# Performance work log

Hardware: AMD Instinct MI355X
Metric: run time of the kernel (lower is better)

## Reference

```python
import jax, jax.numpy as jnp
import numpy as np

KMAX = 192  # static upper bound on sampled subset size k (E[k]~116, std~10 for our vals)


def _dpp_sample(vals, vecs, seed):
    """Sequential DPP sampling (Hough et al. algorithm), jit-compatible via
    fixed-width column padding (KMAX) and lax.while_loop over the k iterations.
    The original's nested classical Gram-Schmidt re-orthonormalization is
    expressed as a QR factorization with the R-diagonal sign convention of GS."""
    n = vals.shape[0]
    key = jax.random.key(seed)
    k_idx, k_loop = jax.random.split(key)

    # Bernoulli selection of eigenvectors: rand(n) < vals/(vals+1)
    index = jax.random.uniform(k_idx, (n,)) < vals / (vals + 1.0)
    k = jnp.sum(index.astype(jnp.int32))
    kk = jnp.minimum(k, KMAX)

    # Pack selected eigenvector columns to the left (stable sort: True first)
    order = jnp.argsort(~index)
    colmask0 = (jnp.arange(KMAX) < kk).astype(vals.dtype)
    V0 = vecs[:, order[:KMAX]] * colmask0[None, :]  # [n, KMAX]

    cols = jnp.arange(KMAX)

    def cond(st):
        i, V, subset = st
        return i < kk

    def body(st):
        i, V, subset = st
        m = kk - i  # number of active columns
        # p_i = ||V[i,:]||^2 over active columns (inactive cols are zero)
        p = jnp.sum(V * V, axis=1)
        c = jnp.cumsum(p / jnp.sum(p))
        u = jax.random.uniform(jax.random.fold_in(k_loop, i))
        item = jnp.argmax(u < c)  # first index where cdf exceeds u
        subset = subset.at[item].set(jnp.asarray(1.0, subset.dtype))
        # first active column j with |V[item, j]| > 0
        jmask = (jnp.abs(V[item]) > 0) & (cols < m)
        j = jnp.argmax(jmask)
        Vj = V[:, j]
        # delete column j (shift left), shrink active width to m-1
        src = jnp.minimum(jnp.where(cols >= j, cols + 1, cols), KMAX - 1)
        newmask = (cols < (m - 1)).astype(V.dtype)
        Vd = V[:, src] * newmask[None, :]
        # eliminate: V <- V - Vj * V[item,:] / Vj[item]
        Ve = (Vd - jnp.outer(Vj, Vd[item] / Vj[item])) * newmask[None, :]
        # re-orthonormalize active columns (classical GS == QR with positive R diag)
        Q, R = jnp.linalg.qr(Ve)
        d = jnp.diagonal(R)
        Q = Q * jnp.where(d >= 0, 1.0, -1.0)[None, :]
        Vn = Q * newmask[None, :]
        Vn = jnp.where(m > 1, Vn, V)  # original skips update when V has 1 column
        return (i + 1, Vn, subset)

    subset0 = jnp.zeros((n,), vals.dtype)
    _, _, subset = jax.lax.while_loop(cond, body, (jnp.int32(0), V0, subset0))
    # original returns all-ones when every eigenvector is selected
    return jnp.where(k == n, jnp.ones((n,), vals.dtype), subset)


def setup_inputs() -> dict:
    key = jax.random.key(0)
    k1, k2 = jax.random.split(key)
    n = 2048
    # eigenvalues in (0.01, 0.11) so E[|subset|] ~ 0.054*n ~ 116 << KMAX
    e = jax.random.uniform(k1, (n,), jnp.float32) * 0.1 + 0.01
    # orthonormal eigenvectors (proper eigendecomposition of a DPP kernel)
    v = jnp.linalg.qr(jax.random.normal(k2, (n, n), jnp.float32))[0]
    return {"e": e, "v": v, "seed": 0}


def reference(e, v, seed):
    return _dpp_sample(e, v, seed)
```

## Files before the change

kernel.cpp:

```cpp
#include <hip/hip_runtime.h>
#include <hip/hip_fp16.h>
#include <stdint.h>
#include <stddef.h>

#define N 2048
#define KMX 192
#define NTH 1024

typedef _Float16 f16x2 __attribute__((ext_vector_type(2)));
typedef _Float16 f16x4 __attribute__((ext_vector_type(4)));

#if defined(__has_builtin)
#if __has_builtin(__builtin_amdgcn_fdot2)
#define HAS_FDOT2 1
#endif
#endif

__device__ __forceinline__ f16x2 bch2(unsigned u) { return __builtin_bit_cast(f16x2, u); }
__device__ __forceinline__ unsigned packh2(float a, float b) {
  unsigned ua = (unsigned)__half_as_ushort(__float2half(a));
  unsigned ub = (unsigned)__half_as_ushort(__float2half(b));
  return ua | (ub << 16);
}
__device__ __forceinline__ float dot2acc(unsigned c, unsigned y, float acc) {
#ifdef HAS_FDOT2
  return __builtin_amdgcn_fdot2(bch2(c), bch2(y), acc, false);
#else
  f16x2 cv = bch2(c), yv = bch2(y);
  acc = fmaf((float)cv[0], (float)yv[0], acc);
  acc = fmaf((float)cv[1], (float)yv[1], acc);
  return acc;
#endif
}

__device__ __forceinline__ void tfround(unsigned &x0, unsigned &x1, const int d) {
  x0 += x1;
  x1 = (x1 << d) | (x1 >> (32 - d));
  x1 ^= x0;
}

__device__ __forceinline__ uint2 tf2x32(unsigned k0, unsigned k1, unsigned c0, unsigned c1) {
  unsigned ks2 = k0 ^ k1 ^ 0x1BD11BDAu;
  unsigned x0 = c0 + k0, x1 = c1 + k1;
  tfround(x0,x1,13); tfround(x0,x1,15); tfround(x0,x1,26); tfround(x0,x1,6);
  x0 += k1;  x1 += ks2 + 1u;
  tfround(x0,x1,17); tfround(x0,x1,29); tfround(x0,x1,16); tfround(x0,x1,24);
  x0 += ks2; x1 += k0 + 2u;
  tfround(x0,x1,13); tfround(x0,x1,15); tfround(x0,x1,26); tfround(x0,x1,6);
  x0 += k0;  x1 += k1 + 3u;
  tfround(x0,x1,17); tfround(x0,x1,29); tfround(x0,x1,16); tfround(x0,x1,24);
  x0 += k1;  x1 += ks2 + 4u;
  tfround(x0,x1,13); tfround(x0,x1,15); tfround(x0,x1,26); tfround(x0,x1,6);
  x0 += ks2; x1 += k0 + 5u;
  uint2 r; r.x = x0; r.y = x1;
  return r;
}

__device__ __forceinline__ float u01(unsigned bits) {
  return __uint_as_float((bits >> 9) | 0x3f800000u) - 1.0f;
}

__global__ void k_select(const float* __restrict__ e, const int* __restrict__ seedp,
                         int* __restrict__ hdr, int* __restrict__ sel) {
  __shared__ unsigned kx0, kx1;
  __shared__ int cnt_s[256];
  __shared__ int pre_s[256];
  const int tid = threadIdx.x;
  if (tid == 0) {
    unsigned seed = (unsigned)seedp[0];
    uint2 kidx  = tf2x32(0u, seed, 0u, 0u);
    uint2 kloop = tf2x32(0u, seed, 0u, 1u);
    kx0 = kidx.x; kx1 = kidx.y;
    hdr[2] = (int)kloop.x;
    hdr[3] = (int)kloop.y;
  }
  __syncthreads();
  const unsigned a0 = kx0, a1 = kx1;
  int flags = 0;
  #pragma unroll
  for (int r = 0; r < 8; ++r) {
    const int i = tid * 8 + r;
    uint2 o = tf2x32(a0, a1, 0u, (unsigned)i);
    float u = u01(o.x ^ o.y);
    float ev = e[i];
    float thr = ev / (ev + 1.0f);
    if (u < thr) flags |= (1 << r);
  }
  cnt_s[tid] = __popc(flags);
  __syncthreads();
  if (tid == 0) {
    int acc = 0;
    for (int t2 = 0; t2 < 256; ++t2) { pre_s[t2] = acc; acc += cnt_s[t2]; }
    hdr[1] = acc;
    hdr[0] = acc < KMX ? acc : KMX;
  }
  __syncthreads();
  int off = pre_s[tid];
  #pragma unroll
  for (int r = 0; r < 8; ++r) {
    if (flags & (1 << r)) {
      if (off < KMX) sel[off] = tid * 8 + r;
      ++off;
    }
  }
}

__global__ void k_gather_h(const float* __restrict__ v, const int* __restrict__ hdr,
                           const int* __restrict__ sel, __half* __restrict__ Gh) {
  const int j = blockIdx.y;
  const int i = blockIdx.x * 256 + threadIdx.x;
  float val = 0.f;
  if (j < hdr[0]) val = v[(size_t)i * N + sel[j]];
  Gh[j * N + i] = __float2half(val);
}

__global__ void k_gather(const float* __restrict__ v, const int* __restrict__ hdr,
                         const int* __restrict__ sel, float* __restrict__ G,
                         __half* __restrict__ Gh) {
  const int j = blockIdx.y;
  const int i = blockIdx.x * 256 + threadIdx.x;
  float val = 0.f;
  if (j < hdr[0]) val = v[(size_t)i * N + sel[j]];
  G[j * N + i] = val;
  Gh[j * N + i] = __float2half(val);
}

__global__ void __launch_bounds__(256)
k_gram(const __half* __restrict__ Gh, const int* __restrict__ hdr,
       __half* __restrict__ Kh) {
  __shared__ __align__(16) __half As[32][64];
  __shared__ __align__(16) __half Bs[32][64];
  const int tid = threadIdx.x;
  const int i0 = blockIdx.y * 64;
  const int i1 = blockIdx.x * 64;
  const int tr = tid & 15, tc = tid >> 4;
  const int kk = hdr[0];
  int kc = (kk + 31) & ~31;
  if (kc > KMX) kc = KMX;

  float acc[4][4];
  #pragma unroll
  for (int r = 0; r < 4; ++r)
    #pragma unroll
    for (int c = 0; c < 4; ++c) acc[r][c] = 0.f;

  const int jr = tid >> 3, c8 = (tid & 7) * 8;
  for (int j0 = 0; j0 < kc; j0 += 32) {
    *(uint4*)&As[jr][c8] = *(const uint4*)(Gh + (size_t)(j0 + jr) * N + i0 + c8);
    *(uint4*)&Bs[jr][c8] = *(const uint4*)(Gh + (size_t)(j0 + jr) * N + i1 + c8);
    __syncthreads();
    #pragma unroll 8
    for (int k = 0; k < 32; ++k) {
      f16x4 a4 = *(const f16x4*)&As[k][tr * 4];
      f16x4 b4 = *(const f16x4*)&Bs[k][tc * 4];
      #pragma unroll
      for (int r = 0; r < 4; ++r)
        #pragma unroll
        for (int c = 0; c < 4; ++c)
          acc[r][c] = fmaf((float)a4[r], (float)b4[c], acc[r][c]);
    }
    __syncthreads();
  }
  #pragma unroll
  for (int r = 0; r < 4; ++r) {
    const int row = i0 + tr * 4 + r;
    uint2 w;
    w.x = packh2(acc[r][0], acc[r][1]);
    w.y = packh2(acc[r][2], acc[r][3]);
    *(uint2*)(Kh + (size_t)row * N + i1 + tc * 4) = w;
  }
}

__global__ void __launch_bounds__(NTH)
k_dpp_chol(const int* __restrict__ hdr, const __half* __restrict__ Kh,
           uint2* __restrict__ YQ, float* __restrict__ out) {
  __shared__ float p_s[N];
  __shared__ uint2 cpack_s[KMX / 4];
  __shared__ float u_s[KMX];
  __shared__ float wsum_s[16];
  __shared__ int item_sh;

  const int tid  = threadIdx.x;
  const int lane = tid & 63;
  const int wave = tid >> 6;
  const int kk    = hdr[0];
  const int kfull = hdr[1];
  const unsigned kl0 = (unsigned)hdr[2];
  const unsigned kl1 = (unsigned)hdr[3];

  const float fill = (kfull == N) ? 1.0f : 0.0f;
  out[tid] = fill;
  out[tid + NTH] = fill;
  if (kfull == N || kk == 0) return;

  const int i0 = 2 * tid;

  float p0 = (float)Kh[(size_t)i0 * N + i0];
  float p1 = (float)Kh[(size_t)(i0 + 1) * N + i0 + 1];
  p_s[i0]     = p0;
  p_s[i0 + 1] = p1;
  if (tid < KMX) {
    uint2 fk = tf2x32(kl0, kl1, 0u, (unsigned)tid);
    uint2 ob = tf2x32(fk.x, fk.y, 0u, 0u);
    u_s[tid] = u01(ob.x ^ ob.y);
  }
  if (tid == 0) item_sh = N;
  __syncthreads();

  for (int t = 0; t < kk; ++t) {
    float ts = p0 + p1;
    float ws = ts;
    #pragma unroll
    for (int d = 1; d < 64; d <<= 1) {
      float o = __shfl_up(ws, d, 64);
      if (lane >= d) ws += o;
    }
    if (lane == 63) wsum_s[wave] = ws;
    __syncthreads();
    float wv = (lane < 16) ? wsum_s[lane] : 0.f;
    #pragma unroll
    for (int d = 1; d < 16; d <<= 1) {
      float o = __shfl_up(wv, d, 16);
      if ((lane & 15) >= d) wv += o;
    }
    const float S    = __shfl(wv, 15, 64);
    const float binc = __shfl(wv, wave, 64);
    const float base_wave = binc - wsum_s[wave];
    const float Sinv = 1.0f / S;
    const float u = u_s[t];
    float excl = __shfl_up(ws, 1, 64);
    if (lane == 0) excl = 0.f;
    const float base = base_wave + excl;
    const float c0 = (base + p0) * Sinv;
    const float c1 = (base + ts) * Sinv;
    const bool m0 = (u < c0);
    const bool m1 = (u < c1);
    unsigned long long bal = __ballot(m0 || m1);
    if (bal) {
      int first = (int)__builtin_ctzll(bal);
      if (lane == first) atomicMin(&item_sh, m0 ? i0 : i0 + 1);
    }
    __syncthreads();
    int item = item_sh;
    if (item >= N) item = 0;
    if (tid == 0) out[item] = 1.0f;
    if (t == kk - 1) break;

    const unsigned kp = *(const unsigned*)(Kh + (size_t)item * N + i0);
    const float rinv = 1.0f / sqrtf(fmaxf(p_s[item], 1e-30f));

    if (tid * 4 < t) {
      uint2 cu = YQ[(size_t)tid * N + item];
      const int rem2 = t - 4 * tid;
      if (rem2 < 4) {
        if (rem2 == 1)      { cu.x &= 0x0000FFFFu; cu.y = 0u; }
        else if (rem2 == 2) { cu.y = 0u; }
        else                { cu.y &= 0x0000FFFFu; }
      }
      cpack_s[tid] = cu;
    }
    if (tid == 0) item_sh = N;
    __syncthreads();

    {
      const int nq = (t + 3) >> 2;
      float acc0 = 0.f, acc1 = 0.f;
      const uint2* Yp = YQ + i0;
      #pragma unroll 4
      for (int q = 0; q < nq; ++q) {
        uint2 cs = cpack_s[q];
        uint4 yv = *(const uint4*)(Yp + (size_t)q * N);
        acc0 = dot2acc(cs.x, yv.x, acc0);
        acc0 = dot2acc(cs.y, yv.y, acc0);
        acc1 = dot2acc(cs.x, yv.z, acc1);
        acc1 = dot2acc(cs.y, yv.w, acc1);
      }
      f16x2 kv = bch2(kp);
      const float y0 = ((float)kv[0] - acc0) * rinv;
      const float y1 = ((float)kv[1] - acc1) * rinv;
      p0 = fmaxf(p0 - y0 * y0, 0.f);
      p1 = fmaxf(p1 - y1 * y1, 0.f);
      p_s[i0]     = p0;
      p_s[i0 + 1] = p1;
      unsigned short* Ys = (unsigned short*)YQ;
      const int rem = t & 3;
      const size_t eb = ((size_t)(t >> 2) * N + i0) * 4;
      Ys[eb + rem]     = __half_as_ushort(__float2half(y0));
      Ys[eb + 4 + rem] = __half_as_ushort(__float2half(y1));
    }
  }
}

__global__ void __launch_bounds__(NTH)
k_dpp_main(const int* __restrict__ hdr, const float* __restrict__ G,
           const __half* __restrict__ Gh, float* __restrict__ D,
           float* __restrict__ out) {
  __shared__ float p_s[N];
  __shared__ float g_s[KMX];
  __shared__ float part[16 * KMX];
  __shared__ float u_s[KMX];
  __shared__ float wsum_s[16];
  __shared__ int item_sh;

  const int tid  = threadIdx.x;
  const int lane = tid & 63;
  const int wave = tid >> 6;
  const int kk    = hdr[0];
  const int kfull = hdr[1];
  const unsigned kl0 = (unsigned)hdr[2];
  const unsigned kl1 = (unsigned)hdr[3];

  const float fill = (kfull == N) ? 1.0f : 0.0f;
  out[tid] = fill;
  out[tid + NTH] = fill;
  if (kfull == N || kk == 0) return;

  const int kkr = (kk + 15) & ~15;

  {
    float s0a = 0.f, s0b = 0.f, s1a = 0.f, s1b = 0.f;
    const __half* base = Gh + 2 * tid;
    for (int j = 0; j < kkr; j += 4) {
      float2 f0 = __half22float2(*(const __half2*)(base + (j + 0) * N));
      float2 f1 = __half22float2(*(const __half2*)(base + (j + 1) * N));
      float2 f2 = __half22float2(*(const __half2*)(base + (j + 2) * N));
      float2 f3 = __half22float2(*(const __half2*)(base + (j + 3) * N));
      s0a = fmaf(f0.x, f0.x, s0a); s1a = fmaf(f0.y, f0.y, s1a);
      s0b = fmaf(f1.x, f1.x, s0b); s1b = fmaf(f1.y, f1.y, s1b);
      s0a = fmaf(f2.x, f2.x, s0a); s1a = fmaf(f2.y, f2.y, s1a);
      s0b = fmaf(f3.x, f3.x, s0b); s1b = fmaf(f3.y, f3.y, s1b);
    }
    p_s[2 * tid]     = s0a + s0b;
    p_s[2 * tid + 1] = s1a + s1b;
    if (tid < KMX) {
      uint2 fk = tf2x32(kl0, kl1, 0u, (unsigned)tid);
      uint2 ob = tf2x32(fk.x, fk.y, 0u, 0u);
      u_s[tid] = u01(ob.x ^ ob.y);
    }
    if (tid == 0) item_sh = N;
  }
  __syncthreads();

  for (int t = 0; t < kk; ++t) {
    float a  = p_s[2 * tid];
    float b  = p_s[2 * tid + 1];
    float ts = a + b;
    float ws = ts;
    #pragma unroll
    for (int d = 1; d < 64; d <<= 1) {
      float o = __shfl_up(ws, d, 64);
      if (lane >= d) ws += o;
    }
    if (lane == 63) wsum_s[wave] = ws;
    __syncthreads();
    float S = 0.f, base_wave = 0.f;
    #pragma unroll
    for (int w = 0; w < 16; ++w) {
      float wv = wsum_s[w];
      if (w < wave) base_wave += wv;
      S += wv;
    }
    const float u = u_s[t];
    float excl = __shfl_up(ws, 1, 64);
    if (lane == 0) excl = 0.f;
    const float base = base_wave + excl;
    const float c0 = (base + a) / S;
    const float c1 = (base + ts) / S;
    const bool m0 = (u < c0);
    const bool m1 = (u < c1);
    unsigned long long bal = __ballot(m0 || m1);
    if (bal) {
      int first = (int)__builtin_ctzll(bal);
      if (lane == first) atomicMin(&item_sh, m0 ? 2 * tid : 2 * tid + 1);
    }
    __syncthreads();
    int item = item_sh;
    if (item >= N) item = 0;
    if (tid == 0) out[item] = 1.0f;
    if (t == kk - 1) break;

    if (tid < KMX) g_s[tid] = G[tid * N + item];
    __syncthreads();

    {
      float g0 = g_s[lane], g1 = g_s[lane + 64], g2 = g_s[lane + 128];
      float a0 = 0.f, a1 = 0.f, a2 = 0.f;
      for (int s = wave; s < t; s += 16) {
        const float* Dr = D + s * KMX;
        float d0 = Dr[lane], d1 = Dr[lane + 64], d2 = Dr[lane + 128];
        float acc = fmaf(d0, g0, fmaf(d1, g1, d2 * g2));
        #pragma unroll
        for (int m = 1; m < 64; m <<= 1) acc += __shfl_xor(acc, m, 64);
        a0 = fmaf(acc, d0, a0); a1 = fmaf(acc, d1, a1); a2 = fmaf(acc, d2, a2);
      }
      part[wave * KMX + lane]       = a0;
      part[wave * KMX + lane + 64]  = a1;
      part[wave * KMX + lane + 128] = a2;
    }
    __syncthreads();
    if (tid < KMX) {
      float gg = g_s[tid];
      #pragma unroll
      for (int w = 0; w < 16; ++w) gg -= part[w * KMX + tid];
      g_s[tid] = gg;
    }
    __syncthreads();

    float gg2 = 0.f;
    {
      float g0 = g_s[lane], g1 = g_s[lane + 64], g2 = g_s[lane + 128];
      float a0 = 0.f, a1 = 0.f, a2 = 0.f;
      for (int s = wave; s < t; s += 16) {
        const float* Dr = D + s * KMX;
        float d0 = Dr[lane], d1 = Dr[lane + 64], d2 = Dr[lane + 128];
        float acc = fmaf(d0, g0, fmaf(d1, g1, d2 * g2));
        #pragma unroll
        for (int m = 1; m < 64; m <<= 1) acc += __shfl_xor(acc, m, 64);
        a0 = fmaf(acc, d0, a0); a1 = fmaf(acc, d1, a1); a2 = fmaf(acc, d2, a2);
      }
      part[wave * KMX + lane]       = a0;
      part[wave * KMX + lane + 64]  = a1;
      part[wave * KMX + lane + 128] = a2;
    }
    __syncthreads();
    if (tid < KMX) {
      float gg = g_s[tid];
      #pragma unroll
      for (int w = 0; w < 16; ++w) gg -= part[w * KMX + tid];
      gg2 = gg;
    }
    if (wave < 3) {
      float r = gg2 * gg2;
      #pragma unroll
      for (int m = 1; m < 64; m <<= 1) r += __shfl_xor(r, m, 64);
      if (lane == 0) wsum_s[wave] = r;
    }
    __syncthreads();
    const float rho = sqrtf(wsum_s[0] + wsum_s[1] + wsum_s[2]);
    if (tid < KMX) {
      float dj = gg2 / rho;
      g_s[tid] = dj;
      D[t * KMX + tid] = dj;
    }
    if (tid == 0) item_sh = N;
    __syncthreads();

    {
      float s0a = 0.f, s0b = 0.f, s1a = 0.f, s1b = 0.f;
      const __half* base2 = Gh + 2 * tid;
      for (int j = 0; j < kkr; j += 4) {
        float d0 = g_s[j], d1 = g_s[j + 1], d2 = g_s[j + 2], d3 = g_s[j + 3];
        float2 f0 = __half22float2(*(const __half2*)(base2 + (j + 0) * N));
        float2 f1 = __half22float2(*(const __half2*)(base2 + (j + 1) * N));
        float2 f2 = __half22float2(*(const __half2*)(base2 + (j + 2) * N));
        float2 f3 = __half22float2(*(const __half2*)(base2 + (j + 3) * N));
        s0a = fmaf(f0.x, d0, s0a); s1a = fmaf(f0.y, d0, s1a);
        s0b = fmaf(f1.x, d1, s0b); s1b = fmaf(f1.y, d1, s1b);
        s0a = fmaf(f2.x, d2, s0a); s1a = fmaf(f2.y, d2, s1a);
        s0b = fmaf(f3.x, d3, s0b); s1b = fmaf(f3.y, d3, s1b);
      }
      float s0 = s0a + s0b, s1 = s1a + s1b;
      p_s[2 * tid]     = fmaxf(p_s[2 * tid]     - s0 * s0, 0.f);
      p_s[2 * tid + 1] = fmaxf(p_s[2 * tid + 1] - s1 * s1, 0.f);
    }
  }
}

extern "C" void kernel_launch(void* const* d_in, const int* in_sizes, int n_in,
                              void* d_out, int out_size, void* d_ws, size_t ws_size,
                              hipStream_t stream) {
  (void)in_sizes; (void)n_in; (void)out_size;
  const float* e    = (const float*)d_in[0];
  const float* v    = (const float*)d_in[1];
  const int*   seed = (const int*)d_in[2];
  float* out = (float*)d_out;

  int* hdr = (int*)d_ws;
  int* sel = hdr + 8;

  if (ws_size >= (size_t)12 * 1024 * 1024) {
    __half* Gh = (__half*)((char*)d_ws + 4096);
    uint2*  YQ = (uint2*)((char*)d_ws + (size_t)2560 * 1024);
    __half* Kh = (__half*)((char*)d_ws + (size_t)4096 * 1024);

    k_select<<<1, 256, 0, stream>>>(e, seed, hdr, sel);
    k_gather_h<<<dim3(8, KMX), 256, 0, stream>>>(v, hdr, sel, Gh);
    k_gram<<<dim3(32, 32), 256, 0, stream>>>(Gh, hdr, Kh);
    k_dpp_chol<<<1, NTH, 0, stream>>>(hdr, Kh, YQ, out);
  } else {
    float*  D  = (float*)((char*)d_ws + 1024);
    float*  G  = (float*)((char*)d_ws + (size_t)256 * 1024);
    __half* Gh = (__half*)((char*)d_ws + (size_t)2048 * 1024);

    k_select<<<1, 256, 0, stream>>>(e, seed, hdr, sel);
    k_gather<<<dim3(8, KMX), 256, 0, stream>>>(v, hdr, sel, G, Gh);
    k_dpp_main<<<1, NTH, 0, stream>>>(hdr, G, Gh, D, out);
  }
}
```

Measured before the change: 67.32 us.

## Use MFMA for Gram matrix with transposed gather and prefetch Y rows

```diff
diff --git a/kernel.cpp b/kernel.cpp
--- a/kernel.cpp
+++ b/kernel.cpp
@@ -6,22 +6,22 @@
 #define N 2048
 #define KMX 192
 #define NTH 1024
+#define PF 12
 
 typedef _Float16 f16x2 __attribute__((ext_vector_type(2)));
-typedef _Float16 f16x4 __attribute__((ext_vector_type(4)));
+typedef _Float16 f16x8 __attribute__((ext_vector_type(8)));
+typedef float f32x4 __attribute__((ext_vector_type(4)));
 
 #if defined(__has_builtin)
 #if __has_builtin(__builtin_amdgcn_fdot2)
 #define HAS_FDOT2 1
 #endif
+#if __has_builtin(__builtin_amdgcn_mfma_f32_16x16x32_f16)
+#define HAS_MFMA16 1
 #endif
+#endif
 
 __device__ __forceinline__ f16x2 bch2(unsigned u) { return __builtin_bit_cast(f16x2, u); }
-__device__ __forceinline__ unsigned packh2(float a, float b) {
-  unsigned ua = (unsigned)__half_as_ushort(__float2half(a));
-  unsigned ub = (unsigned)__half_as_ushort(__float2half(b));
-  return ua | (ub << 16);
-}
 __device__ __forceinline__ float dot2acc(unsigned c, unsigned y, float acc) {
 #ifdef HAS_FDOT2
   return __builtin_amdgcn_fdot2(bch2(c), bch2(y), acc, false);
@@ -105,13 +105,13 @@
   }
 }
 
-__global__ void k_gather_h(const float* __restrict__ v, const int* __restrict__ hdr,
-                           const int* __restrict__ sel, __half* __restrict__ Gh) {
+__global__ void k_gather_t(const float* __restrict__ v, const int* __restrict__ hdr,
+                           const int* __restrict__ sel, __half* __restrict__ GhT) {
   const int j = blockIdx.y;
   const int i = blockIdx.x * 256 + threadIdx.x;
   float val = 0.f;
   if (j < hdr[0]) val = v[(size_t)i * N + sel[j]];
-  Gh[j * N + i] = __float2half(val);
+  GhT[(size_t)i * KMX + j] = __float2half(val);
 }
 
 __global__ void k_gather(const float* __restrict__ v, const int* __restrict__ hdr,
@@ -126,49 +126,53 @@
 }
 
 __global__ void __launch_bounds__(256)
-k_gram(const __half* __restrict__ Gh, const int* __restrict__ hdr,
-       __half* __restrict__ Kh) {
-  __shared__ __align__(16) __half As[32][64];
-  __shared__ __align__(16) __half Bs[32][64];
+k_gram_t(const __half* __restrict__ GhT, __half* __restrict__ Kh) {
+#ifdef HAS_MFMA16
   const int tid = threadIdx.x;
-  const int i0 = blockIdx.y * 64;
-  const int i1 = blockIdx.x * 64;
-  const int tr = tid & 15, tc = tid >> 4;
-  const int kk = hdr[0];
-  int kc = (kk + 31) & ~31;
-  if (kc > KMX) kc = KMX;
-
-  float acc[4][4];
+  const int l = tid & 63;
+  const int w = tid >> 6;
+  const int rowBase = blockIdx.y * 64 + w * 16;
+  const int colBase = blockIdx.x * 64;
+  const int lr = l & 15;
+  const int kg = (l >> 4) * 8;
+  f32x4 acc0 = {0.f,0.f,0.f,0.f}, acc1 = {0.f,0.f,0.f,0.f};
+  f32x4 acc2 = {0.f,0.f,0.f,0.f}, acc3 = {0.f,0.f,0.f,0.f};
+  const __half* Ar = GhT + (size_t)(rowBase + lr) * KMX + kg;
+  const __half* Br = GhT + (size_t)(colBase + lr) * KMX + kg;
   #pragma unroll
-  for (int r = 0; r < 4; ++r)
-    #pragma unroll
-    for (int c = 0; c < 4; ++c) acc[r][c] = 0.f;
-
-  const int jr = tid >> 3, c8 = (tid & 7) * 8;
-  for (int j0 = 0; j0 < kc; j0 += 32) {
-    *(uint4*)&As[jr][c8] = *(const uint4*)(Gh + (size_t)(j0 + jr) * N + i0 + c8);
-    *(uint4*)&Bs[jr][c8] = *(const uint4*)(Gh + (size_t)(j0 + jr) * N + i1 + c8);
-    __syncthreads();
-    #pragma unroll 8
-    for (int k = 0; k < 32; ++k) {
-      f16x4 a4 = *(const f16x4*)&As[k][tr * 4];
-      f16x4 b4 = *(const f16x4*)&Bs[k][tc * 4];
-      #pragma unroll
-      for (int r = 0; r < 4; ++r)
-        #pragma unroll
-        for (int c = 0; c < 4; ++c)
-          acc[r][c] = fmaf((float)a4[r], (float)b4[c], acc[r][c]);
-    }
-    __syncthreads();
-  }
+  for (int j0 = 0; j0 < KMX; j0 += 32) {
+    f16x8 a  = *(const f16x8*)(Ar + j0);
+    f16x8 b0 = *(const f16x8*)(Br + j0);
+    f16x8 b1 = *(const f16x8*)(Br + 16 * KMX + j0);
+    f16x8 b2 = *(const f16x8*)(Br + 32 * KMX + j0);
+    f16x8 b3 = *(const f16x8*)(Br + 48 * KMX + j0);
+    acc0 = __builtin_amdgcn_mfma_f32_16x16x32_f16(a, b0, acc0, 0, 0, 0);
+    acc1 = __builtin_amdgcn_mfma_f32_16x16x32_f16(a, b1, acc1, 0, 0, 0);
+    acc2 = __builtin_amdgcn_mfma_f32_16x16x32_f16(a, b2, acc2, 0, 0, 0);
+    acc3 = __builtin_amdgcn_mfma_f32_16x16x32_f16(a, b3, acc3, 0, 0, 0);
+  }
+  const int orow = rowBase + (l >> 4) * 4;
   #pragma unroll
   for (int r = 0; r < 4; ++r) {
-    const int row = i0 + tr * 4 + r;
-    uint2 w;
-    w.x = packh2(acc[r][0], acc[r][1]);
-    w.y = packh2(acc[r][2], acc[r][3]);
-    *(uint2*)(Kh + (size_t)row * N + i1 + tc * 4) = w;
-  }
+    __half* Kr = Kh + (size_t)(orow + r) * N + colBase + lr;
+    Kr[0]  = __float2half(acc0[r]);
+    Kr[16] = __float2half(acc1[r]);
+    Kr[32] = __float2half(acc2[r]);
+    Kr[48] = __float2half(acc3[r]);
+  }
+#else
+  const int tid = threadIdx.x;
+  const int r0 = blockIdx.y * 64 + (tid & 15) * 4;
+  const int c0 = blockIdx.x * 64 + (tid >> 4) * 4;
+  for (int r = 0; r < 4; ++r)
+    for (int c = 0; c < 4; ++c) {
+      float acc = 0.f;
+      for (int j = 0; j < KMX; ++j)
+        acc = fmaf(__half2float(GhT[(size_t)(r0 + r) * KMX + j]),
+                   __half2float(GhT[(size_t)(c0 + c) * KMX + j]), acc);
+      Kh[(size_t)(r0 + r) * N + c0 + c] = __float2half(acc);
+    }
+#endif
 }
 
 __global__ void __launch_bounds__(NTH)
@@ -248,6 +252,12 @@
 
     const unsigned kp = *(const unsigned*)(Kh + (size_t)item * N + i0);
     const float rinv = 1.0f / sqrtf(fmaxf(p_s[item], 1e-30f));
+    const int nq = (t + 3) >> 2;
+    const uint2* Yp = YQ + i0;
+    uint4 pf[PF];
+    #pragma unroll
+    for (int q = 0; q < PF; ++q)
+      if (q < nq) pf[q] = *(const uint4*)(Yp + (size_t)q * N);
 
     if (tid * 4 < t) {
       uint2 cu = YQ[(size_t)tid * N + item];
@@ -263,11 +273,20 @@
     __syncthreads();
 
     {
-      const int nq = (t + 3) >> 2;
+      const int npf = nq < PF ? nq : PF;
       float acc0 = 0.f, acc1 = 0.f;
-      const uint2* Yp = YQ + i0;
-      #pragma unroll 4
-      for (int q = 0; q < nq; ++q) {
+      #pragma unroll
+      for (int q = 0; q < PF; ++q) {
+        if (q < npf) {
+          uint2 cs = cpack_s[q];
+          uint4 yv = pf[q];
+          acc0 = dot2acc(cs.x, yv.x, acc0);
+          acc0 = dot2acc(cs.y, yv.y, acc0);
+          acc1 = dot2acc(cs.x, yv.z, acc1);
+          acc1 = dot2acc(cs.y, yv.w, acc1);
+        }
+      }
+      for (int q = PF; q < nq; ++q) {
         uint2 cs = cpack_s[q];
         uint4 yv = *(const uint4*)(Yp + (size_t)q * N);
         acc0 = dot2acc(cs.x, yv.x, acc0);
@@ -479,13 +498,13 @@
   int* sel = hdr + 8;
 
   if (ws_size >= (size_t)12 * 1024 * 1024) {
-    __half* Gh = (__half*)((char*)d_ws + 4096);
-    uint2*  YQ = (uint2*)((char*)d_ws + (size_t)2560 * 1024);
-    __half* Kh = (__half*)((char*)d_ws + (size_t)4096 * 1024);
+    __half* GhT = (__half*)((char*)d_ws + 4096);
+    uint2*  YQ  = (uint2*)((char*)d_ws + (size_t)2560 * 1024);
+    __half* Kh  = (__half*)((char*)d_ws + (size_t)4096 * 1024);
 
     k_select<<<1, 256, 0, stream>>>(e, seed, hdr, sel);
-    k_gather_h<<<dim3(8, KMX), 256, 0, stream>>>(v, hdr, sel, Gh);
-    k_gram<<<dim3(32, 32), 256, 0, stream>>>(Gh, hdr, Kh);
+    k_gather_t<<<dim3(8, KMX), 256, 0, stream>>>(v, hdr, sel, GhT);
+    k_gram_t<<<dim3(32, 32), 256, 0, stream>>>(GhT, Kh);
     k_dpp_chol<<<1, NTH, 0, stream>>>(hdr, Kh, YQ, out);
   } else {
     float*  D  = (float*)((char*)d_ws + 1024);
```

Result: slower. 77.83 us (+15.6%).
